# Performance work log

Hardware: AMD Instinct MI355X
Metric: run time of the kernel (lower is better)

Reference implementation:

```python
import jax, jax.numpy as jnp
import numpy as np

B, D, N = 16, 512, 1024


def setup_inputs() -> dict:
    key = jax.random.key(0)
    k1, k2, k3, k4, k5 = jax.random.split(key, 5)
    return {
        "src_embedding": jax.random.normal(k1, (B, D, N), dtype=jnp.float32),
        "tgt_embedding": jax.random.normal(k2, (B, D, N), dtype=jnp.float32),
        "src": jax.random.normal(k3, (B, 3, N), dtype=jnp.float32),
        "tgt": jax.random.normal(k4, (B, 3, N), dtype=jnp.float32),
        "temperature": jax.random.uniform(k5, (B,), dtype=jnp.float32),
    }


def reference(src_embedding, tgt_embedding, src, tgt, temperature):
    b, d, n = src_embedding.shape
    # scores = softmax(temp * (src_emb^T tgt_emb) / sqrt(d_k), dim=2)
    logits = jnp.einsum("bdn,bdm->bnm", src_embedding, tgt_embedding) / np.sqrt(d).astype(np.float32)
    scores = jax.nn.softmax(temperature.reshape(b, 1, 1) * logits, axis=2)  # [B,N,N]
    # src_corr = tgt @ scores^T  -> soft correspondences [B,3,N]
    src_corr = jnp.einsum("bdm,bnm->bdn", tgt, scores)
    src_mean = src.mean(axis=2, keepdims=True)            # [B,3,1]
    corr_mean = src_corr.mean(axis=2, keepdims=True)      # [B,3,1]
    src_c = src - src_mean
    corr_c = src_corr - corr_mean
    H = jnp.einsum("bin,bjn->bij", src_c, corr_c)         # [B,3,3] covariance
    # Kabsch with reflection fix (batched 3x3 SVD)
    u, s, vh = jnp.linalg.svd(H)
    v = jnp.swapaxes(vh, -1, -2)
    ut = jnp.swapaxes(u, -1, -2)
    det = jax.lax.stop_gradient(jnp.linalg.det(v @ ut))   # +/-1, constant in torch (.item())
    d3 = jnp.stack([jnp.ones_like(det), jnp.ones_like(det), det], axis=-1)  # [B,3]
    R = (v * d3[:, None, :]) @ ut                          # v @ diag(1,1,det) @ u^T
    t = (-R @ src_mean) + corr_mean                        # [B,3,1]
    return R, t.reshape(b, 3)
```

## Files before the change

### kernel.cpp

```cpp
#include <hip/hip_runtime.h>
#include <math.h>

#define BATCH 16
#define DIM 512
#define NPTS 1024

typedef __attribute__((ext_vector_type(8))) short short8;
typedef __attribute__((ext_vector_type(4))) float f32x4;

__device__ __forceinline__ unsigned short f2bf(float x) {
    unsigned u = __float_as_uint(x);
    unsigned r = (u + 0x7FFFu + ((u >> 16) & 1u)) >> 16;
    return (unsigned short)r;
}

__device__ __forceinline__ void load_lds16(const void* g, void* l) {
    __builtin_amdgcn_global_load_lds(
        (const __attribute__((address_space(1))) void*)g,
        (__attribute__((address_space(3))) void*)l, 16, 0, 0);
}

__device__ void kabsch_from_H(double H[3][3], const double sm[3], const double cm[3],
                              float* out, int b) {
    double C[3][3];
    for (int i = 0; i < 3; ++i)
        for (int j = 0; j < 3; ++j) {
            double s = 0;
            for (int k = 0; k < 3; ++k) s += H[k][i] * H[k][j];
            C[i][j] = s;
        }
    double V[3][3] = {{1, 0, 0}, {0, 1, 0}, {0, 0, 1}};
    for (int sweep = 0; sweep < 30; ++sweep) {
        const double offd = fabs(C[0][1]) + fabs(C[0][2]) + fabs(C[1][2]);
        const double diag = fabs(C[0][0]) + fabs(C[1][1]) + fabs(C[2][2]);
        if (offd <= 1e-15 * (diag + 1e-300)) break;
        for (int pq = 0; pq < 3; ++pq) {
            const int p = (pq == 2) ? 1 : 0;
            const int q = (pq == 0) ? 1 : 2;
            const double apq = C[p][q];
            if (fabs(apq) < 1e-300) continue;
            const double theta = (C[q][q] - C[p][p]) / (2.0 * apq);
            const double t_ = copysign(1.0, theta) / (fabs(theta) + sqrt(1.0 + theta * theta));
            const double c_ = 1.0 / sqrt(1.0 + t_ * t_);
            const double s_ = t_ * c_;
            const int r = 3 - p - q;
            const double cpp = C[p][p], cqq = C[q][q];
            C[p][p] = cpp - t_ * apq;
            C[q][q] = cqq + t_ * apq;
            C[p][q] = C[q][p] = 0.0;
            const double crp = C[r][p], crq = C[r][q];
            C[r][p] = C[p][r] = c_ * crp - s_ * crq;
            C[r][q] = C[q][r] = s_ * crp + c_ * crq;
            for (int k = 0; k < 3; ++k) {
                const double vkp = V[k][p], vkq = V[k][q];
                V[k][p] = c_ * vkp - s_ * vkq;
                V[k][q] = s_ * vkp + c_ * vkq;
            }
        }
    }
    double lam[3] = {C[0][0], C[1][1], C[2][2]};
    int i0 = 0, i1 = 1, i2 = 2, tswp;
    if (lam[i0] < lam[i1]) { tswp = i0; i0 = i1; i1 = tswp; }
    if (lam[i0] < lam[i2]) { tswp = i0; i0 = i2; i2 = tswp; }
    if (lam[i1] < lam[i2]) { tswp = i1; i1 = i2; i2 = tswp; }

    const double v0[3] = {V[0][i0], V[1][i0], V[2][i0]};
    const double v1[3] = {V[0][i1], V[1][i1], V[2][i1]};
    const double v2[3] = {V[0][i2], V[1][i2], V[2][i2]};
    const double detV = v0[0] * (v1[1] * v2[2] - v1[2] * v2[1])
                      - v0[1] * (v1[0] * v2[2] - v1[2] * v2[0])
                      + v0[2] * (v1[0] * v2[1] - v1[1] * v2[0]);

    double u0[3], u1[3], u2[3];
    for (int i = 0; i < 3; ++i)
        u0[i] = H[i][0] * v0[0] + H[i][1] * v0[1] + H[i][2] * v0[2];
    double n0 = sqrt(u0[0] * u0[0] + u0[1] * u0[1] + u0[2] * u0[2]);
    n0 = fmax(n0, 1e-300);
    u0[0] /= n0; u0[1] /= n0; u0[2] /= n0;
    for (int i = 0; i < 3; ++i)
        u1[i] = H[i][0] * v1[0] + H[i][1] * v1[1] + H[i][2] * v1[2];
    const double d01 = u0[0] * u1[0] + u0[1] * u1[1] + u0[2] * u1[2];
    u1[0] -= d01 * u0[0]; u1[1] -= d01 * u0[1]; u1[2] -= d01 * u0[2];
    double n1 = sqrt(u1[0] * u1[0] + u1[1] * u1[1] + u1[2] * u1[2]);
    n1 = fmax(n1, 1e-300);
    u1[0] /= n1; u1[1] /= n1; u1[2] /= n1;
    u2[0] = u0[1] * u1[2] - u0[2] * u1[1];
    u2[1] = u0[2] * u1[0] - u0[0] * u1[2];
    u2[2] = u0[0] * u1[1] - u0[1] * u1[0];

    double R[3][3];
    for (int a = 0; a < 3; ++a)
        for (int c = 0; c < 3; ++c)
            R[a][c] = v0[a] * u0[c] + v1[a] * u1[c] + detV * v2[a] * u2[c];

    for (int a = 0; a < 3; ++a) {
        const double tv = cm[a] - (R[a][0] * sm[0] + R[a][1] * sm[1] + R[a][2] * sm[2]);
        out[b * 9 + a * 3 + 0] = (float)R[a][0];
        out[b * 9 + a * 3 + 1] = (float)R[a][1];
        out[b * 9 + a * 3 + 2] = (float)R[a][2];
        out[BATCH * 9 + b * 3 + a] = (float)tv;
    }
}

__global__ __launch_bounds__(256) void transpose_bf16_kernel(
    const float* __restrict__ src_emb, const float* __restrict__ tgt_emb,
    unsigned short* __restrict__ AT, unsigned short* __restrict__ BT)
{
    const int bid = blockIdx.x;
    const int pass = bid & 1;
    const int r2 = bid >> 1;
    const int b  = r2 >> 7;
    const int dt = (r2 >> 4) & 7;
    const int nt = r2 & 15;
    const int tid = threadIdx.x;

    __shared__ float tile[64][65];

    const float* src = pass ? tgt_emb : src_emb;
    unsigned short* dst = pass ? BT : AT;

    const int lr = tid >> 4;
    const int c4 = (tid & 15) * 4;
#pragma unroll
    for (int q = 0; q < 4; ++q) {
        const int dl = lr + q * 16;
        const float4 v = *(const float4*)(src + ((size_t)(b * DIM + dt * 64 + dl)) * NPTS + nt * 64 + c4);
        tile[dl][c4 + 0] = v.x;
        tile[dl][c4 + 1] = v.y;
        tile[dl][c4 + 2] = v.z;
        tile[dl][c4 + 3] = v.w;
    }
    __syncthreads();

#pragma unroll
    for (int s = 0; s < 2; ++s) {
        const int nl = s * 32 + (tid >> 3);
        const int d8 = (tid & 7) * 8;
        union { unsigned short us[8]; uint4 q4; } pk;
#pragma unroll
        for (int k = 0; k < 8; ++k) pk.us[k] = f2bf(tile[d8 + k][nl]);
        *(uint4*)(dst + ((size_t)(b * NPTS + nt * 64 + nl)) * DIM + dt * 64 + d8) = pk.q4;
    }
}

#define AB_BYTES 4096
#define BB_BYTES 16384

__global__ __launch_bounds__(256, 2) void attn_corr_kernel(
    const unsigned short* __restrict__ AT, const unsigned short* __restrict__ BT,
    const float* __restrict__ tgt, const float* __restrict__ temperature,
    float* __restrict__ P)
{
    __shared__ char lds[4 * (AB_BYTES + BB_BYTES)];

    const int bid = blockIdx.x;
    const int slice = bid & 7;
    const int j     = bid >> 3;
    const int pair  = j >> 4;
    const int qt    = j & 15;
    const int pidx  = slice * 8 + pair;
    const int b     = pidx >> 2;
    const int ms    = pidx & 3;

    const int tid = threadIdx.x;
    const int lane = tid & 63;
    const int wv = tid >> 6;

    const unsigned short* Abase = AT + ((size_t)b * NPTS + qt * 64) * DIM;
    const unsigned short* Bbase = BT + ((size_t)b * NPTS + ms * 256) * DIM;

    const int a_r  = wv * 16 + (lane >> 2);
    const int a_cl = (lane & 3) ^ ((a_r >> 1) & 3);
    const size_t a_src_off = (size_t)a_r * DIM + a_cl * 8;

    int b_r[4], b_cl[4];
#pragma unroll
    for (int q = 0; q < 4; ++q) {
        b_r[q]  = q * 64 + wv * 16 + (lane >> 2);
        b_cl[q] = (lane & 3) ^ ((b_r[q] >> 1) & 3);
    }

    const int fp = lane & 15;
    const int fg = lane >> 4;

    const float s2 = temperature[b] * (0.04419417382415922f * 1.4426950408889634f);
    const float* tb = tgt + (size_t)b * 3 * NPTS;
    float tv0[4][4], tv1[4][4], tv2[4][4];
#pragma unroll
    for (int kt = 0; kt < 4; ++kt)
#pragma unroll
        for (int reg = 0; reg < 4; ++reg) {
            const int m = ms * 256 + wv * 64 + kt * 16 + fg * 4 + reg;
            tv0[kt][reg] = tb[m];
            tv1[kt][reg] = tb[NPTS + m];
            tv2[kt][reg] = tb[2 * NPTS + m];
        }
    __builtin_amdgcn_sched_barrier(0);

    f32x4 acc[4][4];
#pragma unroll
    for (int kt = 0; kt < 4; ++kt)
#pragma unroll
        for (int qj = 0; qj < 4; ++qj) acc[kt][qj] = (f32x4){0.f, 0.f, 0.f, 0.f};

    char* AbP[4] = {lds, lds + AB_BYTES, lds + 2 * AB_BYTES, lds + 3 * AB_BYTES};
    char* BbP[4] = {lds + 4 * AB_BYTES,
                    lds + 4 * AB_BYTES + BB_BYTES,
                    lds + 4 * AB_BYTES + 2 * BB_BYTES,
                    lds + 4 * AB_BYTES + 3 * BB_BYTES};

#define STAGE(CH, ABUF, BBUF)                                                        \
    {                                                                                \
        const int d0_ = (CH) * 32;                                                   \
        load_lds16(Abase + a_src_off + d0_, (ABUF) + wv * 1024);                     \
        _Pragma("unroll")                                                            \
        for (int q = 0; q < 4; ++q)                                                  \
            load_lds16(Bbase + (size_t)b_r[q] * DIM + d0_ + b_cl[q] * 8,             \
                       (BBUF) + q * 4096 + wv * 1024);                               \
    }

#define COMPUTE(ABUF, BBUF)                                                          \
    {                                                                                \
        short8 kf[4], qf[4];                                                         \
        _Pragma("unroll")                                                            \
        for (int kt = 0; kt < 4; ++kt) {                                             \
            const int r = wv * 64 + kt * 16 + fp;                                    \
            const int cl = fg ^ ((r >> 1) & 3);                                      \
            kf[kt] = *(const short8*)((BBUF) + r * 64 + cl * 16);                    \
        }                                                                            \
        _Pragma("unroll")                                                            \
        for (int qj = 0; qj < 4; ++qj) {                                             \
            const int r = qj * 16 + fp;                                              \
            const int cl = fg ^ ((r >> 1) & 3);                                      \
            qf[qj] = *(const short8*)((ABUF) + r * 64 + cl * 16);                    \
        }                                                                            \
        __builtin_amdgcn_s_setprio(1);                                               \
        _Pragma("unroll")                                                            \
        for (int kt = 0; kt < 4; ++kt)                                               \
            _Pragma("unroll")                                                        \
            for (int qj = 0; qj < 4; ++qj)                                           \
                acc[kt][qj] = __builtin_amdgcn_mfma_f32_16x16x32_bf16(               \
                    kf[kt], qf[qj], acc[kt][qj], 0, 0, 0);                           \
        __builtin_amdgcn_s_setprio(0);                                               \
    }

    STAGE(0, AbP[0], BbP[0]);
    STAGE(1, AbP[1], BbP[1]);
    STAGE(2, AbP[2], BbP[2]);

#pragma unroll
    for (int ch = 0; ch < 16; ++ch) {
        if (ch <= 13)      { asm volatile("s_waitcnt vmcnt(10)" ::: "memory"); }
        else if (ch == 14) { asm volatile("s_waitcnt vmcnt(5)"  ::: "memory"); }
        else               { asm volatile("s_waitcnt vmcnt(0)"  ::: "memory"); }
        __builtin_amdgcn_s_barrier();
        __builtin_amdgcn_sched_barrier(0);
        if (ch + 3 < 16) STAGE(ch + 3, AbP[(ch + 3) & 3], BbP[(ch + 3) & 3]);
        COMPUTE(AbP[ch & 3], BbP[ch & 3]);
        __builtin_amdgcn_sched_barrier(0);
    }

    float l[4]  = {0.f, 0.f, 0.f, 0.f};
    float a0[4] = {0.f, 0.f, 0.f, 0.f};
    float a1[4] = {0.f, 0.f, 0.f, 0.f};
    float a2[4] = {0.f, 0.f, 0.f, 0.f};

#pragma unroll
    for (int kt = 0; kt < 4; ++kt) {
#pragma unroll
        for (int qj = 0; qj < 4; ++qj) {
#pragma unroll
            for (int reg = 0; reg < 4; ++reg) {
                const float w = exp2f(acc[kt][qj][reg] * s2);
                l[qj]  += w;
                a0[qj] = fmaf(w, tv0[kt][reg], a0[qj]);
                a1[qj] = fmaf(w, tv1[kt][reg], a1[qj]);
                a2[qj] = fmaf(w, tv2[kt][reg], a2[qj]);
            }
        }
    }

    float* Pb = P + ((size_t)b * 16 + (ms * 4 + wv)) * 4 * NPTS;
#pragma unroll
    for (int qj = 0; qj < 4; ++qj) {
        float lv = l[qj], v0 = a0[qj], v1 = a1[qj], v2 = a2[qj];
        lv += __shfl_xor(lv, 16); lv += __shfl_xor(lv, 32);
        v0 += __shfl_xor(v0, 16); v0 += __shfl_xor(v0, 32);
        v1 += __shfl_xor(v1, 16); v1 += __shfl_xor(v1, 32);
        v2 += __shfl_xor(v2, 16); v2 += __shfl_xor(v2, 32);
        if (fg == 0) {
            const int n = qt * 64 + qj * 16 + fp;
            Pb[0 * NPTS + n] = lv;
            Pb[1 * NPTS + n] = v0;
            Pb[2 * NPTS + n] = v1;
            Pb[3 * NPTS + n] = v2;
        }
    }
}

__global__ __launch_bounds__(256) void merge_reduce_svd_kernel(
    const float* __restrict__ P, const float* __restrict__ src,
    float* __restrict__ out)
{
    const int b = blockIdx.x;
    const int tid = threadIdx.x;

    __shared__ float wred[4][9];
    __shared__ float meansh[6];

    float corr[4][3], sv[4][3];
    float cs0 = 0, cs1 = 0, cs2 = 0, ss0 = 0, ss1 = 0, ss2 = 0;

#pragma unroll
    for (int j = 0; j < 4; ++j) {
        const int n = tid + j * 256;
        float l = 0, a0 = 0, a1 = 0, a2 = 0;
        for (int pp = 0; pp < 16; ++pp) {
            const float* Pb = P + ((size_t)b * 16 + pp) * 4 * NPTS;
            l  += Pb[n];
            a0 += Pb[NPTS + n];
            a1 += Pb[2 * NPTS + n];
            a2 += Pb[3 * NPTS + n];
        }
        const float inv = 1.0f / l;
        corr[j][0] = a0 * inv; corr[j][1] = a1 * inv; corr[j][2] = a2 * inv;
        cs0 += corr[j][0]; cs1 += corr[j][1]; cs2 += corr[j][2];
        sv[j][0] = src[((size_t)b * 3 + 0) * NPTS + n];
        sv[j][1] = src[((size_t)b * 3 + 1) * NPTS + n];
        sv[j][2] = src[((size_t)b * 3 + 2) * NPTS + n];
        ss0 += sv[j][0]; ss1 += sv[j][1]; ss2 += sv[j][2];
    }

#pragma unroll
    for (int off = 1; off < 64; off <<= 1) {
        ss0 += __shfl_xor(ss0, off); ss1 += __shfl_xor(ss1, off); ss2 += __shfl_xor(ss2, off);
        cs0 += __shfl_xor(cs0, off); cs1 += __shfl_xor(cs1, off); cs2 += __shfl_xor(cs2, off);
    }
    const int wave = tid >> 6;
    if ((tid & 63) == 0) {
        wred[wave][0] = ss0; wred[wave][1] = ss1; wred[wave][2] = ss2;
        wred[wave][3] = cs0; wred[wave][4] = cs1; wred[wave][5] = cs2;
    }
    __syncthreads();
    if (tid < 6)
        meansh[tid] = (wred[0][tid] + wred[1][tid] + wred[2][tid] + wred[3][tid]) * (1.0f / NPTS);
    __syncthreads();
    const float sm0 = meansh[0], sm1 = meansh[1], sm2 = meansh[2];
    const float cm0 = meansh[3], cm1 = meansh[4], cm2 = meansh[5];

    float h[9] = {0, 0, 0, 0, 0, 0, 0, 0, 0};
#pragma unroll
    for (int j = 0; j < 4; ++j) {
        const float a0 = sv[j][0] - sm0, a1 = sv[j][1] - sm1, a2 = sv[j][2] - sm2;
        const float b0 = corr[j][0] - cm0, b1 = corr[j][1] - cm1, b2 = corr[j][2] - cm2;
        h[0] += a0 * b0; h[1] += a0 * b1; h[2] += a0 * b2;
        h[3] += a1 * b0; h[4] += a1 * b1; h[5] += a1 * b2;
        h[6] += a2 * b0; h[7] += a2 * b1; h[8] += a2 * b2;
    }
#pragma unroll
    for (int off = 1; off < 64; off <<= 1) {
#pragma unroll
        for (int j = 0; j < 9; ++j) h[j] += __shfl_xor(h[j], off);
    }
    __syncthreads();
    if ((tid & 63) == 0) {
#pragma unroll
        for (int j = 0; j < 9; ++j) wred[wave][j] = h[j];
    }
    __syncthreads();

    if (tid == 0) {
        double H[3][3];
        for (int i = 0; i < 3; ++i)
            for (int j = 0; j < 3; ++j)
                H[i][j] = (double)wred[0][i * 3 + j] + wred[1][i * 3 + j]
                        + wred[2][i * 3 + j] + wred[3][i * 3 + j];
        const double sm[3] = {sm0, sm1, sm2};
        const double cm[3] = {cm0, cm1, cm2};
        kabsch_from_H(H, sm, cm, out, b);
    }
}

__global__ __launch_bounds__(256) void flash_corr_kernel(
    const float* __restrict__ src_emb,
    const float* __restrict__ tgt_emb,
    const float* __restrict__ tgt,
    const float* __restrict__ temperature,
    float* __restrict__ corr)
{
    const int bid = blockIdx.x;
    const int b   = bid & 15;
    const int qt  = bid >> 4;
    const int n0  = qt * 64;
    const int tid = threadIdx.x;
    const int tx  = tid & 15;
    const int ty  = tid >> 4;

    const float scale = temperature[b] * (1.0f / sqrtf((float)DIM));

    __shared__ float As[2][32][64];
    __shared__ float Bs[2][32][64];
    __shared__ float Ts[3][64];

    const float* Abase  = src_emb + (size_t)b * DIM * NPTS + n0;
    const float* Bbatch = tgt_emb + (size_t)b * DIM * NPTS;
    const float* Tbatch = tgt     + (size_t)b * 3 * NPTS;

    const int dr0 = tid >> 4;
    const int dr1 = dr0 + 16;
    const int c4  = (tid & 15) * 4;

    float mrun[4], lpart[4], acc0[4], acc1[4], acc2[4];
#pragma unroll
    for (int r = 0; r < 4; ++r) {
        mrun[r] = -1e30f; lpart[r] = 0.0f;
        acc0[r] = 0.0f; acc1[r] = 0.0f; acc2[r] = 0.0f;
    }

    for (int mt = 0; mt < 16; ++mt) {
        const int m0 = mt * 64;
        const float* Bbase = Bbatch + m0;
        __syncthreads();
        if (tid < 192) {
            const int i = tid >> 6, mc = tid & 63;
            Ts[i][mc] = Tbatch[i * NPTS + m0 + mc];
        }
        {
            float4 a0 = *(const float4*)(Abase + (size_t)dr0 * NPTS + c4);
            float4 a1 = *(const float4*)(Abase + (size_t)dr1 * NPTS + c4);
            float4 b0 = *(const float4*)(Bbase + (size_t)dr0 * NPTS + c4);
            float4 b1 = *(const float4*)(Bbase + (size_t)dr1 * NPTS + c4);
            *(float4*)&As[0][dr0][c4] = a0;
            *(float4*)&As[0][dr1][c4] = a1;
            *(float4*)&Bs[0][dr0][c4] = b0;
            *(float4*)&Bs[0][dr1][c4] = b1;
        }
        __syncthreads();

        float S[4][4];
#pragma unroll
        for (int r = 0; r < 4; ++r)
#pragma unroll
            for (int c = 0; c < 4; ++c) S[r][c] = 0.0f;

        for (int ch = 0; ch < 16; ++ch) {
            const int buf = ch & 1;
            float4 a0n, a1n, b0n, b1n;
            if (ch < 15) {
                const float* Ab = Abase + (size_t)(ch + 1) * 32 * NPTS;
                const float* Bb = Bbase + (size_t)(ch + 1) * 32 * NPTS;
                a0n = *(const float4*)(Ab + (size_t)dr0 * NPTS + c4);
                a1n = *(const float4*)(Ab + (size_t)dr1 * NPTS + c4);
                b0n = *(const float4*)(Bb + (size_t)dr0 * NPTS + c4);
                b1n = *(const float4*)(Bb + (size_t)dr1 * NPTS + c4);
            }
#pragma unroll
            for (int dk = 0; dk < 32; ++dk) {
                const float4 av = *(const float4*)(&As[buf][dk][ty * 4]);
                const float4 bv = *(const float4*)(&Bs[buf][dk][tx * 4]);
                S[0][0] = fmaf(av.x, bv.x, S[0][0]);
                S[0][1] = fmaf(av.x, bv.y, S[0][1]);
                S[0][2] = fmaf(av.x, bv.z, S[0][2]);
                S[0][3] = fmaf(av.x, bv.w, S[0][3]);
                S[1][0] = fmaf(av.y, bv.x, S[1][0]);
                S[1][1] = fmaf(av.y, bv.y, S[1][1]);
                S[1][2] = fmaf(av.y, bv.z, S[1][2]);
                S[1][3] = fmaf(av.y, bv.w, S[1][3]);
                S[2][0] = fmaf(av.z, bv.x, S[2][0]);
                S[2][1] = fmaf(av.z, bv.y, S[2][1]);
                S[2][2] = fmaf(av.z, bv.z, S[2][2]);
                S[2][3] = fmaf(av.z, bv.w, S[2][3]);
                S[3][0] = fmaf(av.w, bv.x, S[3][0]);
                S[3][1] = fmaf(av.w, bv.y, S[3][1]);
                S[3][2] = fmaf(av.w, bv.z, S[3][2]);
                S[3][3] = fmaf(av.w, bv.w, S[3][3]);
            }
            __syncthreads();
            if (ch < 15) {
                *(float4*)&As[buf ^ 1][dr0][c4] = a0n;
                *(float4*)&As[buf ^ 1][dr1][c4] = a1n;
                *(float4*)&Bs[buf ^ 1][dr0][c4] = b0n;
                *(float4*)&Bs[buf ^ 1][dr1][c4] = b1n;
                __syncthreads();
            }
        }

#pragma unroll
        for (int r = 0; r < 4; ++r) {
            float z0 = S[r][0] * scale, z1 = S[r][1] * scale;
            float z2 = S[r][2] * scale, z3 = S[r][3] * scale;
            float mt_ = fmaxf(fmaxf(z0, z1), fmaxf(z2, z3));
#pragma unroll
            for (int off = 1; off < 16; off <<= 1)
                mt_ = fmaxf(mt_, __shfl_xor(mt_, off));
            const float mnew = fmaxf(mrun[r], mt_);
            const float f = expf(mrun[r] - mnew);
            lpart[r] *= f; acc0[r] *= f; acc1[r] *= f; acc2[r] *= f;
            const float w0 = expf(z0 - mnew);
            const float w1 = expf(z1 - mnew);
            const float w2 = expf(z2 - mnew);
            const float w3 = expf(z3 - mnew);
            lpart[r] += w0 + w1 + w2 + w3;
            const int mc = tx * 4;
            acc0[r] += w0 * Ts[0][mc] + w1 * Ts[0][mc+1] + w2 * Ts[0][mc+2] + w3 * Ts[0][mc+3];
            acc1[r] += w0 * Ts[1][mc] + w1 * Ts[1][mc+1] + w2 * Ts[1][mc+2] + w3 * Ts[1][mc+3];
            acc2[r] += w0 * Ts[2][mc] + w1 * Ts[2][mc+1] + w2 * Ts[2][mc+2] + w3 * Ts[2][mc+3];
            mrun[r] = mnew;
        }
    }

#pragma unroll
    for (int r = 0; r < 4; ++r) {
        float l = lpart[r], a0 = acc0[r], a1 = acc1[r], a2 = acc2[r];
#pragma unroll
        for (int off = 1; off < 16; off <<= 1) {
            l  += __shfl_xor(l,  off);
            a0 += __shfl_xor(a0, off);
            a1 += __shfl_xor(a1, off);
            a2 += __shfl_xor(a2, off);
        }
        if (tx == 0) {
            const int n = n0 + ty * 4 + r;
            const float inv = 1.0f / l;
            corr[((size_t)b * 3 + 0) * NPTS + n] = a0 * inv;
            corr[((size_t)b * 3 + 1) * NPTS + n] = a1 * inv;
            corr[((size_t)b * 3 + 2) * NPTS + n] = a2 * inv;
        }
    }
}

__global__ __launch_bounds__(256) void reduce_svd_kernel(
    const float* __restrict__ src,
    const float* __restrict__ corr,
    float* __restrict__ out)
{
    const int b = blockIdx.x;
    const int tid = threadIdx.x;

    __shared__ float wred[4][9];
    __shared__ float meansh[6];

    const float* sp = src  + (size_t)b * 3 * NPTS;
    const float* cp = corr + (size_t)b * 3 * NPTS;

    float ss0 = 0, ss1 = 0, ss2 = 0, cs0 = 0, cs1 = 0, cs2 = 0;
    for (int n = tid; n < NPTS; n += 256) {
        ss0 += sp[n]; ss1 += sp[NPTS + n]; ss2 += sp[2 * NPTS + n];
        cs0 += cp[n]; cs1 += cp[NPTS + n]; cs2 += cp[2 * NPTS + n];
    }
#pragma unroll
    for (int off = 1; off < 64; off <<= 1) {
        ss0 += __shfl_xor(ss0, off); ss1 += __shfl_xor(ss1, off); ss2 += __shfl_xor(ss2, off);
        cs0 += __shfl_xor(cs0, off); cs1 += __shfl_xor(cs1, off); cs2 += __shfl_xor(cs2, off);
    }
    const int wave = tid >> 6;
    if ((tid & 63) == 0) {
        wred[wave][0] = ss0; wred[wave][1] = ss1; wred[wave][2] = ss2;
        wred[wave][3] = cs0; wred[wave][4] = cs1; wred[wave][5] = cs2;
    }
    __syncthreads();
    if (tid < 6)
        meansh[tid] = (wred[0][tid] + wred[1][tid] + wred[2][tid] + wred[3][tid]) * (1.0f / NPTS);
    __syncthreads();
    const float sm0 = meansh[0], sm1 = meansh[1], sm2 = meansh[2];
    const float cm0 = meansh[3], cm1 = meansh[4], cm2 = meansh[5];

    float h[9] = {0, 0, 0, 0, 0, 0, 0, 0, 0};
    for (int n = tid; n < NPTS; n += 256) {
        const float a0 = sp[n] - sm0, a1 = sp[NPTS + n] - sm1, a2 = sp[2 * NPTS + n] - sm2;
        const float b0 = cp[n] - cm0, b1 = cp[NPTS + n] - cm1, b2 = cp[2 * NPTS + n] - cm2;
        h[0] += a0 * b0; h[1] += a0 * b1; h[2] += a0 * b2;
        h[3] += a1 * b0; h[4] += a1 * b1; h[5] += a1 * b2;
        h[6] += a2 * b0; h[7] += a2 * b1; h[8] += a2 * b2;
    }
#pragma unroll
    for (int off = 1; off < 64; off <<= 1) {
#pragma unroll
        for (int j = 0; j < 9; ++j) h[j] += __shfl_xor(h[j], off);
    }
    __syncthreads();
    if ((tid & 63) == 0) {
#pragma unroll
        for (int j = 0; j < 9; ++j) wred[wave][j] = h[j];
    }
    __syncthreads();

    if (tid == 0) {
        double H[3][3];
        for (int i = 0; i < 3; ++i)
            for (int j = 0; j < 3; ++j)
                H[i][j] = (double)wred[0][i * 3 + j] + wred[1][i * 3 + j]
                        + wred[2][i * 3 + j] + wred[3][i * 3 + j];
        const double sm[3] = {sm0, sm1, sm2};
        const double cm[3] = {cm0, cm1, cm2};
        kabsch_from_H(H, sm, cm, out, b);
    }
}

extern "C" void kernel_launch(void* const* d_in, const int* in_sizes, int n_in,
                              void* d_out, int out_size, void* d_ws, size_t ws_size,
                              hipStream_t stream) {
    const float* src_emb = (const float*)d_in[0];
    const float* tgt_emb = (const float*)d_in[1];
    const float* src     = (const float*)d_in[2];
    const float* tgt     = (const float*)d_in[3];
    const float* temp    = (const float*)d_in[4];
    float* out = (float*)d_out;

    const size_t AT_BYTES = (size_t)BATCH * NPTS * DIM * 2;
    const size_t P_BYTES  = (size_t)BATCH * 16 * 4 * NPTS * 4;

    if (ws_size >= 2 * AT_BYTES + P_BYTES) {
        unsigned short* AT = (unsigned short*)d_ws;
        unsigned short* BT = (unsigned short*)((char*)d_ws + AT_BYTES);
        float* P = (float*)((char*)d_ws + 2 * AT_BYTES);

        transpose_bf16_kernel<<<dim3(2 * BATCH * 8 * 16), dim3(256), 0, stream>>>(
            src_emb, tgt_emb, AT, BT);
        attn_corr_kernel<<<dim3(BATCH * 16 * 4), dim3(256), 0, stream>>>(
            AT, BT, tgt, temp, P);
        merge_reduce_svd_kernel<<<dim3(BATCH), dim3(256), 0, stream>>>(P, src, out);
    } else {
        float* corr = (float*)d_ws;
        flash_corr_kernel<<<dim3(BATCH * (NPTS / 64)), dim3(256), 0, stream>>>(
            src_emb, tgt_emb, tgt, temp, corr);
        reduce_svd_kernel<<<dim3(BATCH), dim3(256), 0, stream>>>(src, corr, out);
    }
}
```

Before: 58.72 us.

## Pre-swizzle bf16 operands into MFMA fragment layout and drop LDS staging

The transpose kernel now writes the bf16 embeddings in a layout where each 16-row by 32-column MFMA fragment is contiguous, so each lane's operand is one 16-byte load. The attention kernel becomes single-wave blocks that load fragments straight from global memory into registers with double buffering, removing LDS staging, barriers and waitcnt scheduling. This gives four times as many blocks, each computing a 64x64 tile. The trade-off is losing LDS reuse across waves, since each wave re-reads its A fragments from global or L2.

```diff
diff --git a/kernel.cpp b/kernel.cpp
--- a/kernel.cpp
+++ b/kernel.cpp
@@ -12,12 +12,6 @@
     unsigned u = __float_as_uint(x);
     unsigned r = (u + 0x7FFFu + ((u >> 16) & 1u)) >> 16;
     return (unsigned short)r;
-}
-
-__device__ __forceinline__ void load_lds16(const void* g, void* l) {
-    __builtin_amdgcn_global_load_lds(
-        (const __attribute__((address_space(1))) void*)g,
-        (__attribute__((address_space(3))) void*)l, 16, 0, 0);
 }
 
 __device__ void kabsch_from_H(double H[3][3], const double sm[3], const double cm[3],
@@ -111,7 +105,7 @@
     const int r2 = bid >> 1;
     const int b  = r2 >> 7;
     const int dt = (r2 >> 4) & 7;
-    const int nt = r2 & 15;
+    const int nt64 = r2 & 15;
     const int tid = threadIdx.x;
 
     __shared__ float tile[64][65];
@@ -124,7 +118,7 @@
 #pragma unroll
     for (int q = 0; q < 4; ++q) {
         const int dl = lr + q * 16;
-        const float4 v = *(const float4*)(src + ((size_t)(b * DIM + dt * 64 + dl)) * NPTS + nt * 64 + c4);
+        const float4 v = *(const float4*)(src + ((size_t)(b * DIM + dt * 64 + dl)) * NPTS + nt64 * 64 + c4);
         tile[dl][c4 + 0] = v.x;
         tile[dl][c4 + 1] = v.y;
         tile[dl][c4 + 2] = v.z;
@@ -132,132 +126,101 @@
     }
     __syncthreads();
 
-#pragma unroll
-    for (int s = 0; s < 2; ++s) {
-        const int nl = s * 32 + (tid >> 3);
-        const int d8 = (tid & 7) * 8;
+    const int w   = tid >> 6;
+    const int fp  = (tid >> 2) & 15;
+    const int fg2 = tid & 3;
+    const int nl  = w * 16 + fp;
+#pragma unroll
+    for (int jj = 0; jj < 2; ++jj) {
+        const int ch = dt * 2 + jj;
+        const int d0 = jj * 32 + fg2 * 8;
         union { unsigned short us[8]; uint4 q4; } pk;
 #pragma unroll
-        for (int k = 0; k < 8; ++k) pk.us[k] = f2bf(tile[d8 + k][nl]);
-        *(uint4*)(dst + ((size_t)(b * NPTS + nt * 64 + nl)) * DIM + dt * 64 + d8) = pk.q4;
-    }
-}
-
-#define AB_BYTES 4096
-#define BB_BYTES 16384
-
-__global__ __launch_bounds__(256, 2) void attn_corr_kernel(
+        for (int k = 0; k < 8; ++k) pk.us[k] = f2bf(tile[d0 + k][nl]);
+        const size_t off = ((size_t)((b * 64 + (nt64 * 4 + w)) * 16 + ch)) * 512
+                         + fp * 32 + fg2 * 8;
+        *(uint4*)(dst + off) = pk.q4;
+    }
+}
+
+__global__ __launch_bounds__(64, 3) void attn_corr_kernel(
     const unsigned short* __restrict__ AT, const unsigned short* __restrict__ BT,
     const float* __restrict__ tgt, const float* __restrict__ temperature,
     float* __restrict__ P)
 {
-    __shared__ char lds[4 * (AB_BYTES + BB_BYTES)];
-
     const int bid = blockIdx.x;
     const int slice = bid & 7;
-    const int j     = bid >> 3;
-    const int pair  = j >> 4;
-    const int qt    = j & 15;
-    const int pidx  = slice * 8 + pair;
-    const int b     = pidx >> 2;
-    const int ms    = pidx & 3;
-
-    const int tid = threadIdx.x;
-    const int lane = tid & 63;
-    const int wv = tid >> 6;
-
-    const unsigned short* Abase = AT + ((size_t)b * NPTS + qt * 64) * DIM;
-    const unsigned short* Bbase = BT + ((size_t)b * NPTS + ms * 256) * DIM;
-
-    const int a_r  = wv * 16 + (lane >> 2);
-    const int a_cl = (lane & 3) ^ ((a_r >> 1) & 3);
-    const size_t a_src_off = (size_t)a_r * DIM + a_cl * 8;
-
-    int b_r[4], b_cl[4];
-#pragma unroll
-    for (int q = 0; q < 4; ++q) {
-        b_r[q]  = q * 64 + wv * 16 + (lane >> 2);
-        b_cl[q] = (lane & 3) ^ ((b_r[q] >> 1) & 3);
-    }
-
+    const int j  = bid >> 3;
+    const int b  = slice * 2 + (j >> 8);
+    const int r  = j & 255;
+    const int qt = r >> 4;
+    const int p  = r & 15;
+
+    const int lane = threadIdx.x;
     const int fp = lane & 15;
     const int fg = lane >> 4;
+    const int voff = fp * 64 + fg * 16;
+
+    const char* Abase = (const char*)AT + ((size_t)b * 64 * 16) * 1024;
+    const char* Bbase = (const char*)BT + ((size_t)b * 64 * 16) * 1024;
+    const char* Aq[4];
+    const char* Bk[4];
+#pragma unroll
+    for (int q = 0; q < 4; ++q) {
+        Aq[q] = Abase + (size_t)(qt * 4 + q) * 16384 + voff;
+        Bk[q] = Bbase + (size_t)(p  * 4 + q) * 16384 + voff;
+    }
+
+    f32x4 acc[4][4];
+#pragma unroll
+    for (int kt = 0; kt < 4; ++kt)
+#pragma unroll
+        for (int qj = 0; qj < 4; ++qj) acc[kt][qj] = (f32x4){0.f, 0.f, 0.f, 0.f};
+
+#define LOADF(QF, KF, CH)                                                      \
+    {                                                                          \
+        _Pragma("unroll")                                                      \
+        for (int q = 0; q < 4; ++q) {                                          \
+            QF[q] = *(const short8*)(Aq[q] + (CH) * 1024);                     \
+            KF[q] = *(const short8*)(Bk[q] + (CH) * 1024);                     \
+        }                                                                      \
+    }
+
+#define MM(QF, KF)                                                             \
+    {                                                                          \
+        __builtin_amdgcn_s_setprio(1);                                         \
+        _Pragma("unroll")                                                      \
+        for (int kt = 0; kt < 4; ++kt)                                         \
+            _Pragma("unroll")                                                  \
+            for (int qj = 0; qj < 4; ++qj)                                     \
+                acc[kt][qj] = __builtin_amdgcn_mfma_f32_16x16x32_bf16(         \
+                    KF[kt], QF[qj], acc[kt][qj], 0, 0, 0);                     \
+        __builtin_amdgcn_s_setprio(0);                                         \
+    }
+
+    short8 qfA[4], kfA[4], qfB[4], kfB[4];
+    LOADF(qfA, kfA, 0);
+#pragma unroll
+    for (int s = 0; s < 8; ++s) {
+        LOADF(qfB, kfB, 2 * s + 1);
+        MM(qfA, kfA);
+        if (s < 7) {
+            LOADF(qfA, kfA, 2 * s + 2);
+            MM(qfB, kfB);
+        } else {
+            MM(qfB, kfB);
+        }
+    }
 
     const float s2 = temperature[b] * (0.04419417382415922f * 1.4426950408889634f);
     const float* tb = tgt + (size_t)b * 3 * NPTS;
-    float tv0[4][4], tv1[4][4], tv2[4][4];
-#pragma unroll
-    for (int kt = 0; kt < 4; ++kt)
-#pragma unroll
-        for (int reg = 0; reg < 4; ++reg) {
-            const int m = ms * 256 + wv * 64 + kt * 16 + fg * 4 + reg;
-            tv0[kt][reg] = tb[m];
-            tv1[kt][reg] = tb[NPTS + m];
-            tv2[kt][reg] = tb[2 * NPTS + m];
-        }
-    __builtin_amdgcn_sched_barrier(0);
-
-    f32x4 acc[4][4];
-#pragma unroll
-    for (int kt = 0; kt < 4; ++kt)
-#pragma unroll
-        for (int qj = 0; qj < 4; ++qj) acc[kt][qj] = (f32x4){0.f, 0.f, 0.f, 0.f};
-
-    char* AbP[4] = {lds, lds + AB_BYTES, lds + 2 * AB_BYTES, lds + 3 * AB_BYTES};
-    char* BbP[4] = {lds + 4 * AB_BYTES,
-                    lds + 4 * AB_BYTES + BB_BYTES,
-                    lds + 4 * AB_BYTES + 2 * BB_BYTES,
-                    lds + 4 * AB_BYTES + 3 * BB_BYTES};
-
-#define STAGE(CH, ABUF, BBUF)                                                        \
-    {                                                                                \
-        const int d0_ = (CH) * 32;                                                   \
-        load_lds16(Abase + a_src_off + d0_, (ABUF) + wv * 1024);                     \
-        _Pragma("unroll")                                                            \
-        for (int q = 0; q < 4; ++q)                                                  \
-            load_lds16(Bbase + (size_t)b_r[q] * DIM + d0_ + b_cl[q] * 8,             \
-                       (BBUF) + q * 4096 + wv * 1024);                               \
-    }
-
-#define COMPUTE(ABUF, BBUF)                                                          \
-    {                                                                                \
-        short8 kf[4], qf[4];                                                         \
-        _Pragma("unroll")                                                            \
-        for (int kt = 0; kt < 4; ++kt) {                                             \
-            const int r = wv * 64 + kt * 16 + fp;                                    \
-            const int cl = fg ^ ((r >> 1) & 3);                                      \
-            kf[kt] = *(const short8*)((BBUF) + r * 64 + cl * 16);                    \
-        }                                                                            \
-        _Pragma("unroll")                                                            \
-        for (int qj = 0; qj < 4; ++qj) {                                             \
-            const int r = qj * 16 + fp;                                              \
-            const int cl = fg ^ ((r >> 1) & 3);                                      \
-            qf[qj] = *(const short8*)((ABUF) + r * 64 + cl * 16);                    \
-        }                                                                            \
-        __builtin_amdgcn_s_setprio(1);                                               \
-        _Pragma("unroll")                                                            \
-        for (int kt = 0; kt < 4; ++kt)                                               \
-            _Pragma("unroll")                                                        \
-            for (int qj = 0; qj < 4; ++qj)                                           \
-                acc[kt][qj] = __builtin_amdgcn_mfma_f32_16x16x32_bf16(               \
-                    kf[kt], qf[qj], acc[kt][qj], 0, 0, 0);                           \
-        __builtin_amdgcn_s_setprio(0);                                               \
-    }
-
-    STAGE(0, AbP[0], BbP[0]);
-    STAGE(1, AbP[1], BbP[1]);
-    STAGE(2, AbP[2], BbP[2]);
-
-#pragma unroll
-    for (int ch = 0; ch < 16; ++ch) {
-        if (ch <= 13)      { asm volatile("s_waitcnt vmcnt(10)" ::: "memory"); }
-        else if (ch == 14) { asm volatile("s_waitcnt vmcnt(5)"  ::: "memory"); }
-        else               { asm volatile("s_waitcnt vmcnt(0)"  ::: "memory"); }
-        __builtin_amdgcn_s_barrier();
-        __builtin_amdgcn_sched_barrier(0);
-        if (ch + 3 < 16) STAGE(ch + 3, AbP[(ch + 3) & 3], BbP[(ch + 3) & 3]);
-        COMPUTE(AbP[ch & 3], BbP[ch & 3]);
-        __builtin_amdgcn_sched_barrier(0);
+    float t0[4][4], t1[4][4], t2[4][4];
+#pragma unroll
+    for (int kt = 0; kt < 4; ++kt) {
+        const int m0 = p * 64 + kt * 16 + fg * 4;
+        *(float4*)t0[kt] = *(const float4*)(tb + m0);
+        *(float4*)t1[kt] = *(const float4*)(tb + NPTS + m0);
+        *(float4*)t2[kt] = *(const float4*)(tb + 2 * NPTS + m0);
     }
 
     float l[4]  = {0.f, 0.f, 0.f, 0.f};
@@ -273,14 +236,14 @@
             for (int reg = 0; reg < 4; ++reg) {
                 const float w = exp2f(acc[kt][qj][reg] * s2);
                 l[qj]  += w;
-                a0[qj] = fmaf(w, tv0[kt][reg], a0[qj]);
-                a1[qj] = fmaf(w, tv1[kt][reg], a1[qj]);
-                a2[qj] = fmaf(w, tv2[kt][reg], a2[qj]);
+                a0[qj] = fmaf(w, t0[kt][reg], a0[qj]);
+                a1[qj] = fmaf(w, t1[kt][reg], a1[qj]);
+                a2[qj] = fmaf(w, t2[kt][reg], a2[qj]);
             }
         }
     }
 
-    float* Pb = P + ((size_t)b * 16 + (ms * 4 + wv)) * 4 * NPTS;
+    float* Pb = P + ((size_t)b * 16 + p) * 4 * NPTS;
 #pragma unroll
     for (int qj = 0; qj < 4; ++qj) {
         float lv = l[qj], v0 = a0[qj], v1 = a1[qj], v2 = a2[qj];
@@ -617,7 +580,7 @@
 
         transpose_bf16_kernel<<<dim3(2 * BATCH * 8 * 16), dim3(256), 0, stream>>>(
             src_emb, tgt_emb, AT, BT);
-        attn_corr_kernel<<<dim3(BATCH * 16 * 4), dim3(256), 0, stream>>>(
+        attn_corr_kernel<<<dim3(BATCH * 16 * 16), dim3(64), 0, stream>>>(
             AT, BT, tgt, temp, P);
         merge_reduce_svd_kernel<<<dim3(BATCH), dim3(256), 0, stream>>>(P, src, out);
     } else {
```

After: 65.61 us. +11.7%, slower.

## Split merge/reduce across 64 blocks and compute covariance from raw moments

Applied to the files above, without the earlier changes.

The single 16-block merge+reduce+SVD kernel is replaced by a 64-block partial kernel and a small final kernel. Each partial block merges the 16 attention partials for 256 points and reduces 15 raw sums (source sums, correspondence sums and their cross products) in one pass. A per-batch thread then builds the covariance in double as the sum of products minus N times the product of the means, and runs Kabsch. This raises parallelism and removes the second pass over the points, but adds a kernel launch and relies on the raw-moment formula, which can lose precision.

```diff
diff --git a/kernel.cpp b/kernel.cpp
--- a/kernel.cpp
+++ b/kernel.cpp
@@ -298,87 +298,72 @@
     }
 }
 
-__global__ __launch_bounds__(256) void merge_reduce_svd_kernel(
+__global__ __launch_bounds__(256) void merge_partial_kernel(
     const float* __restrict__ P, const float* __restrict__ src,
-    float* __restrict__ out)
+    float* __restrict__ Pacc)
+{
+    const int bid = blockIdx.x;
+    const int b   = bid >> 2;
+    const int seg = bid & 3;
+    const int tid = threadIdx.x;
+    const int n   = seg * 256 + tid;
+
+    const float* Pb = P + (size_t)b * 16 * 4 * NPTS;
+    float l = 0, a0 = 0, a1 = 0, a2 = 0;
+    for (int pp = 0; pp < 16; ++pp) {
+        const float* q = Pb + (size_t)pp * 4 * NPTS;
+        l  += q[n];
+        a0 += q[NPTS + n];
+        a1 += q[2 * NPTS + n];
+        a2 += q[3 * NPTS + n];
+    }
+    const float inv = 1.0f / l;
+    const float c0 = a0 * inv, c1 = a1 * inv, c2 = a2 * inv;
+
+    const float* sp = src + (size_t)b * 3 * NPTS;
+    const float s0 = sp[n], s1 = sp[NPTS + n], s2 = sp[2 * NPTS + n];
+
+    float v[15] = { s0, s1, s2, c0, c1, c2,
+                    s0 * c0, s0 * c1, s0 * c2,
+                    s1 * c0, s1 * c1, s1 * c2,
+                    s2 * c0, s2 * c1, s2 * c2 };
+
+#pragma unroll
+    for (int off = 1; off < 64; off <<= 1)
+#pragma unroll
+        for (int k = 0; k < 15; ++k) v[k] += __shfl_xor(v[k], off);
+
+    __shared__ float red[4][15];
+    const int wv = tid >> 6;
+    if ((tid & 63) == 0)
+#pragma unroll
+        for (int k = 0; k < 15; ++k) red[wv][k] = v[k];
+    __syncthreads();
+    if (tid < 15)
+        Pacc[bid * 15 + tid] = red[0][tid] + red[1][tid] + red[2][tid] + red[3][tid];
+}
+
+__global__ __launch_bounds__(64) void svd_final_kernel(
+    const float* __restrict__ Pacc, float* __restrict__ out)
 {
     const int b = blockIdx.x;
-    const int tid = threadIdx.x;
-
-    __shared__ float wred[4][9];
-    __shared__ float meansh[6];
-
-    float corr[4][3], sv[4][3];
-    float cs0 = 0, cs1 = 0, cs2 = 0, ss0 = 0, ss1 = 0, ss2 = 0;
-
-#pragma unroll
-    for (int j = 0; j < 4; ++j) {
-        const int n = tid + j * 256;
-        float l = 0, a0 = 0, a1 = 0, a2 = 0;
-        for (int pp = 0; pp < 16; ++pp) {
-            const float* Pb = P + ((size_t)b * 16 + pp) * 4 * NPTS;
-            l  += Pb[n];
-            a0 += Pb[NPTS + n];
-            a1 += Pb[2 * NPTS + n];
-            a2 += Pb[3 * NPTS + n];
-        }
-        const float inv = 1.0f / l;
-        corr[j][0] = a0 * inv; corr[j][1] = a1 * inv; corr[j][2] = a2 * inv;
-        cs0 += corr[j][0]; cs1 += corr[j][1]; cs2 += corr[j][2];
-        sv[j][0] = src[((size_t)b * 3 + 0) * NPTS + n];
-        sv[j][1] = src[((size_t)b * 3 + 1) * NPTS + n];
-        sv[j][2] = src[((size_t)b * 3 + 2) * NPTS + n];
-        ss0 += sv[j][0]; ss1 += sv[j][1]; ss2 += sv[j][2];
-    }
-
-#pragma unroll
-    for (int off = 1; off < 64; off <<= 1) {
-        ss0 += __shfl_xor(ss0, off); ss1 += __shfl_xor(ss1, off); ss2 += __shfl_xor(ss2, off);
-        cs0 += __shfl_xor(cs0, off); cs1 += __shfl_xor(cs1, off); cs2 += __shfl_xor(cs2, off);
-    }
-    const int wave = tid >> 6;
-    if ((tid & 63) == 0) {
-        wred[wave][0] = ss0; wred[wave][1] = ss1; wred[wave][2] = ss2;
-        wred[wave][3] = cs0; wred[wave][4] = cs1; wred[wave][5] = cs2;
-    }
-    __syncthreads();
-    if (tid < 6)
-        meansh[tid] = (wred[0][tid] + wred[1][tid] + wred[2][tid] + wred[3][tid]) * (1.0f / NPTS);
-    __syncthreads();
-    const float sm0 = meansh[0], sm1 = meansh[1], sm2 = meansh[2];
-    const float cm0 = meansh[3], cm1 = meansh[4], cm2 = meansh[5];
-
-    float h[9] = {0, 0, 0, 0, 0, 0, 0, 0, 0};
-#pragma unroll
-    for (int j = 0; j < 4; ++j) {
-        const float a0 = sv[j][0] - sm0, a1 = sv[j][1] - sm1, a2 = sv[j][2] - sm2;
-        const float b0 = corr[j][0] - cm0, b1 = corr[j][1] - cm1, b2 = corr[j][2] - cm2;
-        h[0] += a0 * b0; h[1] += a0 * b1; h[2] += a0 * b2;
-        h[3] += a1 * b0; h[4] += a1 * b1; h[5] += a1 * b2;
-        h[6] += a2 * b0; h[7] += a2 * b1; h[8] += a2 * b2;
-    }
-#pragma unroll
-    for (int off = 1; off < 64; off <<= 1) {
-#pragma unroll
-        for (int j = 0; j < 9; ++j) h[j] += __shfl_xor(h[j], off);
-    }
-    __syncthreads();
-    if ((tid & 63) == 0) {
-#pragma unroll
-        for (int j = 0; j < 9; ++j) wred[wave][j] = h[j];
-    }
-    __syncthreads();
-
-    if (tid == 0) {
-        double H[3][3];
-        for (int i = 0; i < 3; ++i)
-            for (int j = 0; j < 3; ++j)
-                H[i][j] = (double)wred[0][i * 3 + j] + wred[1][i * 3 + j]
-                        + wred[2][i * 3 + j] + wred[3][i * 3 + j];
-        const double sm[3] = {sm0, sm1, sm2};
-        const double cm[3] = {cm0, cm1, cm2};
-        kabsch_from_H(H, sm, cm, out, b);
-    }
+    if (threadIdx.x != 0) return;
+
+    double s[15];
+    for (int k = 0; k < 15; ++k) {
+        double acc = 0;
+        for (int seg = 0; seg < 4; ++seg)
+            acc += (double)Pacc[(b * 4 + seg) * 15 + k];
+        s[k] = acc;
+    }
+    const double invN = 1.0 / (double)NPTS;
+    const double sm[3] = {s[0] * invN, s[1] * invN, s[2] * invN};
+    const double cm[3] = {s[3] * invN, s[4] * invN, s[5] * invN};
+    double H[3][3];
+    for (int i = 0; i < 3; ++i)
+        for (int jj = 0; jj < 3; ++jj)
+            H[i][jj] = s[6 + i * 3 + jj] - (double)NPTS * sm[i] * cm[jj];
+    kabsch_from_H(H, sm, cm, out, b);
 }
 
 __global__ __launch_bounds__(256) void flash_corr_kernel(
@@ -607,19 +592,22 @@
     const float* temp    = (const float*)d_in[4];
     float* out = (float*)d_out;
 
-    const size_t AT_BYTES = (size_t)BATCH * NPTS * DIM * 2;
-    const size_t P_BYTES  = (size_t)BATCH * 16 * 4 * NPTS * 4;
-
-    if (ws_size >= 2 * AT_BYTES + P_BYTES) {
+    const size_t AT_BYTES   = (size_t)BATCH * NPTS * DIM * 2;
+    const size_t P_BYTES    = (size_t)BATCH * 16 * 4 * NPTS * 4;
+    const size_t PACC_BYTES = 64 * 15 * sizeof(float);
+
+    if (ws_size >= 2 * AT_BYTES + P_BYTES + PACC_BYTES) {
         unsigned short* AT = (unsigned short*)d_ws;
         unsigned short* BT = (unsigned short*)((char*)d_ws + AT_BYTES);
-        float* P = (float*)((char*)d_ws + 2 * AT_BYTES);
+        float* P    = (float*)((char*)d_ws + 2 * AT_BYTES);
+        float* Pacc = (float*)((char*)d_ws + 2 * AT_BYTES + P_BYTES);
 
         transpose_bf16_kernel<<<dim3(2 * BATCH * 8 * 16), dim3(256), 0, stream>>>(
             src_emb, tgt_emb, AT, BT);
         attn_corr_kernel<<<dim3(BATCH * 16 * 4), dim3(256), 0, stream>>>(
             AT, BT, tgt, temp, P);
-        merge_reduce_svd_kernel<<<dim3(BATCH), dim3(256), 0, stream>>>(P, src, out);
+        merge_partial_kernel<<<dim3(64), dim3(256), 0, stream>>>(P, src, Pacc);
+        svd_final_kernel<<<dim3(BATCH), dim3(64), 0, stream>>>(Pacc, out);
     } else {
         float* corr = (float*)d_ws;
         flash_corr_kernel<<<dim3(BATCH * (NPTS / 64)), dim3(256), 0, stream>>>(
```

Result: no change. 58.29 us (-0.7%).
